# Optimization experiments

Measured on AMD Instinct MI355X. Metric: run time of the kernel, lower is better.

Reference implementation:

```python
import jax, jax.numpy as jnp
import numpy as np

H = 128            # hidden_size; also the chunk length from torch.split(x, hidden_size)
NUM_CHUNKS = 4096  # B
INPUT_SIZE = 1
NUM_CLASSES = 1


def setup_inputs() -> dict:
    key = jax.random.key(0)
    ks = jax.random.split(key, 7)
    N = NUM_CHUNKS * H
    s = 1.0 / np.sqrt(H).astype(np.float32)
    x = jax.random.normal(ks[0], (N,), dtype=jnp.float32)
    W_ih = jax.random.uniform(ks[1], (4 * H, INPUT_SIZE), minval=-s, maxval=s, dtype=jnp.float32)
    W_hh = jax.random.uniform(ks[2], (4 * H, H), minval=-s, maxval=s, dtype=jnp.float32)
    b_ih = jax.random.uniform(ks[3], (4 * H,), minval=-s, maxval=s, dtype=jnp.float32)
    b_hh = jax.random.uniform(ks[4], (4 * H,), minval=-s, maxval=s, dtype=jnp.float32)
    fc_W = jax.random.uniform(ks[5], (NUM_CLASSES, H), minval=-s, maxval=s, dtype=jnp.float32)
    fc_b = jax.random.uniform(ks[6], (NUM_CLASSES,), minval=-s, maxval=s, dtype=jnp.float32)
    return {"x": x, "W_ih": W_ih, "W_hh": W_hh, "b_ih": b_ih, "b_hh": b_hh,
            "fc_W": fc_W, "fc_b": fc_b}


def reference(x, W_ih, W_hh, b_ih, b_hh, fc_W, fc_b):
    # Original: split flat x into chunks of length H, run each chunk as a
    # batch-1 LSTM (input_size=1), take final hidden state, apply fc_out.
    # Here all chunks are batched into one fused recurrent pass.
    Hh = W_hh.shape[1]
    xb = x.reshape(-1, Hh, 1)                                  # [B, T=H, 1]
    # input projection is time-parallel: precompute gate pre-activations
    pre = jnp.einsum('bti,gi->btg', xb, W_ih) + b_ih + b_hh    # [B, T, 4H]

    def step(carry, p_t):
        h, c = carry                                           # [B, H] each
        gates = p_t + h @ W_hh.T                               # [B, 4H]
        i, f, g, o = jnp.split(gates, 4, axis=-1)              # PyTorch gate order i,f,g,o
        i = jax.nn.sigmoid(i)
        f = jax.nn.sigmoid(f)
        g = jnp.tanh(g)
        o = jax.nn.sigmoid(o)
        c = f * c + i * g
        h = o * jnp.tanh(c)
        return (h, c), None

    B = xb.shape[0]
    h0 = jnp.zeros((B, Hh), dtype=x.dtype)
    c0 = jnp.zeros((B, Hh), dtype=x.dtype)
    (hT, _), _ = jax.lax.scan(step, (h0, c0), jnp.swapaxes(pre, 0, 1))
    return hT @ fc_W.T + fc_b                                  # [B, num_classes]
```

## Files before the change

### kernel.cpp

```cpp
#include <hip/hip_runtime.h>


#define H   128
#define T   128
#define BLOCK 512
#define HSTRIDE 136
#define XSTRIDE 20
#define LOG2E    1.44269504088896340736f
#define TWOLOG2E 2.88539008177792681472f

typedef _Float16 f16x8 __attribute__((ext_vector_type(8)));
typedef float    f32x4 __attribute__((ext_vector_type(4)));

__global__ void prep_whh_kernel(const float* __restrict__ W_hh, _Float16* __restrict__ wfrag)
{
    int idx = blockIdx.x * blockDim.x + threadIdx.x;
    int l15 =  idx        & 15;
    int q   = (idx >> 4)  & 3;
    int kc  = (idx >> 6)  & 3;
    int g   = (idx >> 8)  & 3;
    int ct  = (idx >> 10) & 7;
    int n  = g * H + ct * 16 + l15;
    int k0 = kc * 32 + q * 8;
    float s = (g == 2) ? TWOLOG2E : LOG2E;
    const float* src = W_hh + (size_t)n * H + k0;
    f16x8 f;
    #pragma unroll
    for (int i = 0; i < 8; ++i) f[i] = (_Float16)(src[i] * s);
    *(f16x8*)(wfrag + (size_t)idx * 8) = f;
}

__device__ __forceinline__ float frcp(float v)  { return __builtin_amdgcn_rcpf(v); }
__device__ __forceinline__ float fexp2(float v) { return __builtin_amdgcn_exp2f(v); }

__device__ __forceinline__ void lstm_step(const _Float16* hr, _Float16* hw,
                                          const float* xp,
                                          const f16x8 wf[4][4],
                                          const float* wihs, const float* biass,
                                          float* c, int l15, int q, int jcol)
{
    const _Float16* ar = hr + l15 * HSTRIDE + q * 8;
    f16x8 af0 = *(const f16x8*)(ar);
    f16x8 af1 = *(const f16x8*)(ar + 32);
    f16x8 af2 = *(const f16x8*)(ar + 64);
    f16x8 af3 = *(const f16x8*)(ar + 96);

    float4 xl = *(const float4*)xp;
    f32x4 acc[4];
    #pragma unroll
    for (int g = 0; g < 4; ++g) {
        f32x4 iv;
        iv[0] = fmaf(xl.x, wihs[g], biass[g]);
        iv[1] = fmaf(xl.y, wihs[g], biass[g]);
        iv[2] = fmaf(xl.z, wihs[g], biass[g]);
        iv[3] = fmaf(xl.w, wihs[g], biass[g]);
        acc[g] = __builtin_amdgcn_mfma_f32_16x16x32_f16(af0, wf[g][0], iv, 0, 0, 0);
    }
    #pragma unroll
    for (int g = 0; g < 4; ++g)
        acc[g] = __builtin_amdgcn_mfma_f32_16x16x32_f16(af1, wf[g][1], acc[g], 0, 0, 0);
    #pragma unroll
    for (int g = 0; g < 4; ++g)
        acc[g] = __builtin_amdgcn_mfma_f32_16x16x32_f16(af2, wf[g][2], acc[g], 0, 0, 0);
    #pragma unroll
    for (int g = 0; g < 4; ++g)
        acc[g] = __builtin_amdgcn_mfma_f32_16x16x32_f16(af3, wf[g][3], acc[g], 0, 0, 0);

    float Ei[4], Ef[4], Eg[4], Eo[4];
    #pragma unroll
    for (int r = 0; r < 4; ++r) {
        Ei[r] = fexp2(-acc[0][r]);
        Ef[r] = fexp2(-acc[1][r]);
        Eg[r] = fexp2( acc[2][r]);
        Eo[r] = fexp2(-acc[3][r]);
    }
    _Float16* hwp = hw + (q * 4) * HSTRIDE + jcol;
    #pragma unroll
    for (int r = 0; r < 4; ++r) {
        float u  = 1.0f + Ei[r];
        float v  = 1.0f + Ef[r];
        float w  = 1.0f + Eg[r];
        float wm = Eg[r] - 1.0f;
        float uw = u * w;
        float cn = fmaf(c[r], uw, wm * v) * frcp(v * uw);
        c[r] = cn;
        float Ec = fexp2(cn * TWOLOG2E);
        float hv = (Ec - 1.0f) * frcp((Ec + 1.0f) * (1.0f + Eo[r]));
        hwp[r * HSTRIDE] = (_Float16)hv;
    }
}

__launch_bounds__(BLOCK, 2)
__global__ void lstm_fused_kernel(const float* __restrict__ x,
                                  const float* __restrict__ W_ih,
                                  const _Float16* __restrict__ wfrag,
                                  const float* __restrict__ b_ih,
                                  const float* __restrict__ b_hh,
                                  const float* __restrict__ fc_W,
                                  const float* __restrict__ fc_b,
                                  float* __restrict__ out)
{
    __shared__ __align__(16) float xs[T][XSTRIDE];
    __shared__ __align__(16) _Float16 hb0[16 * HSTRIDE];
    __shared__ __align__(16) _Float16 hb1[16 * HSTRIDE];

    const int tid  = threadIdx.x;
    const int wave = tid >> 6;
    const int lane = tid & 63;
    const int l15  = lane & 15;
    const int q    = lane >> 4;
    const int jcol = wave * 16 + l15;

    {
        const int t0 = tid & 127;
        const int bb = tid >> 7;
        const float* xb = x + (size_t)blockIdx.x * (16 * T);
        xs[t0][bb]      = xb[bb * T + t0];
        xs[t0][bb + 4]  = xb[(bb + 4) * T + t0];
        xs[t0][bb + 8]  = xb[(bb + 8) * T + t0];
        xs[t0][bb + 12] = xb[(bb + 12) * T + t0];
    }
    for (int i = tid; i < 16 * HSTRIDE; i += BLOCK)
        hb0[i] = (_Float16)0.0f;

    f16x8 wf[4][4];
    float wihs[4], biass[4];
    {
        const _Float16* wbase = wfrag + (size_t)wave * 8192;
        #pragma unroll
        for (int g = 0; g < 4; ++g) {
            const int n = g * H + jcol;
            const float s = (g == 2) ? TWOLOG2E : LOG2E;
            wihs[g]  = W_ih[n] * s;
            biass[g] = (b_ih[n] + b_hh[n]) * s;
            #pragma unroll
            for (int kc = 0; kc < 4; ++kc)
                wf[g][kc] = *(const f16x8*)(wbase + ((((g * 4 + kc) * 4 + q) * 16 + l15) * 8));
        }
    }

    float c[4] = {0.f, 0.f, 0.f, 0.f};
    const float* xp = &xs[0][q * 4];

    __syncthreads();

    #pragma unroll 1
    for (int t2 = 0; t2 < T / 2; ++t2) {
        lstm_step(hb0, hb1, xp, wf, wihs, biass, c, l15, q, jcol);
        xp += XSTRIDE;
        __syncthreads();
        lstm_step(hb1, hb0, xp, wf, wihs, biass, c, l15, q, jcol);
        xp += XSTRIDE;
        __syncthreads();
    }

    if (tid < 256) {
        const int b    = tid >> 4;
        const int part = tid & 15;
        const _Float16* hrow = &hb0[b * HSTRIDE];
        float s = 0.0f;
        #pragma unroll
        for (int i = 0; i < 8; ++i) {
            const int j = part * 8 + i;
            s += fc_W[j] * (float)hrow[j];
        }
        s += __shfl_xor(s, 8, 16);
        s += __shfl_xor(s, 4, 16);
        s += __shfl_xor(s, 2, 16);
        s += __shfl_xor(s, 1, 16);
        if (part == 0)
            out[blockIdx.x * 16 + b] = s + fc_b[0];
    }
}

extern "C" void kernel_launch(void* const* d_in, const int* in_sizes, int n_in,
                              void* d_out, int out_size, void* d_ws, size_t ws_size,
                              hipStream_t stream)
{
    const float* x    = (const float*)d_in[0];
    const float* W_ih = (const float*)d_in[1];
    const float* W_hh = (const float*)d_in[2];
    const float* b_ih = (const float*)d_in[3];
    const float* b_hh = (const float*)d_in[4];
    const float* fc_W = (const float*)d_in[5];
    const float* fc_b = (const float*)d_in[6];
    float* out = (float*)d_out;

    _Float16* wfrag = (_Float16*)d_ws;

    hipLaunchKernelGGL(prep_whh_kernel, dim3(32), dim3(256), 0, stream, W_hh, wfrag);

    const int B = in_sizes[0] / H;
    dim3 grid(B / 16);
    dim3 block(BLOCK);
    hipLaunchKernelGGL(lstm_fused_kernel, grid, block, 0, stream,
                       x, W_ih, wfrag, b_ih, b_hh, fc_W, fc_b, out);
}
```

Baseline: 168.9 us.

## Interleave two 16-sequence cohorts per block to overlap MFMA and gate math

Each block now processes 32 sequences split into two cohorts, A and B, with separate hidden-state buffers and cell states. The recurrence is software-pipelined so the MFMA gate matmul of one cohort is issued next to the elementwise sigmoid/tanh update of the other. The aim is to hide MFMA latency and the barrier behind independent VALU work. In exchange the grid is halved, so with 4096 sequences only 128 blocks launch. That may leave half of the GPU's compute units idle, and per-thread register and LDS use grows.

```diff
diff --git a/kernel.cpp b/kernel.cpp
--- a/kernel.cpp
+++ b/kernel.cpp
@@ -3,9 +3,10 @@
 
 #define H   128
 #define T   128
+#define MB  32
 #define BLOCK 512
 #define HSTRIDE 136
-#define XSTRIDE 20
+#define XSTRIDE 36
 #define LOG2E    1.44269504088896340736f
 #define TWOLOG2E 2.88539008177792681472f
 
@@ -33,11 +34,11 @@
 __device__ __forceinline__ float frcp(float v)  { return __builtin_amdgcn_rcpf(v); }
 __device__ __forceinline__ float fexp2(float v) { return __builtin_amdgcn_exp2f(v); }
 
-__device__ __forceinline__ void lstm_step(const _Float16* hr, _Float16* hw,
-                                          const float* xp,
-                                          const f16x8 wf[4][4],
-                                          const float* wihs, const float* biass,
-                                          float* c, int l15, int q, int jcol)
+__device__ __forceinline__ void mfma_coh(f32x4 acc[4], const _Float16* hr,
+                                         const float* xp,
+                                         const f16x8 wf[4][4],
+                                         const float* wihs, const float* biass,
+                                         int l15, int q)
 {
     const _Float16* ar = hr + l15 * HSTRIDE + q * 8;
     f16x8 af0 = *(const f16x8*)(ar);
@@ -46,7 +47,6 @@
     f16x8 af3 = *(const f16x8*)(ar + 96);
 
     float4 xl = *(const float4*)xp;
-    f32x4 acc[4];
     #pragma unroll
     for (int g = 0; g < 4; ++g) {
         f32x4 iv;
@@ -65,7 +65,11 @@
     #pragma unroll
     for (int g = 0; g < 4; ++g)
         acc[g] = __builtin_amdgcn_mfma_f32_16x16x32_f16(af3, wf[g][3], acc[g], 0, 0, 0);
-
+}
+
+__device__ __forceinline__ void ew_coh(const f32x4 acc[4], float* c, _Float16* hw,
+                                       int q, int jcol)
+{
     float Ei[4], Ef[4], Eg[4], Eo[4];
     #pragma unroll
     for (int r = 0; r < 4; ++r) {
@@ -101,8 +105,8 @@
                                   float* __restrict__ out)
 {
     __shared__ __align__(16) float xs[T][XSTRIDE];
-    __shared__ __align__(16) _Float16 hb0[16 * HSTRIDE];
-    __shared__ __align__(16) _Float16 hb1[16 * HSTRIDE];
+    __shared__ __align__(16) _Float16 hA[16 * HSTRIDE];
+    __shared__ __align__(16) _Float16 hB[16 * HSTRIDE];
 
     const int tid  = threadIdx.x;
     const int wave = tid >> 6;
@@ -113,15 +117,18 @@
 
     {
         const int t0 = tid & 127;
-        const int bb = tid >> 7;
-        const float* xb = x + (size_t)blockIdx.x * (16 * T);
-        xs[t0][bb]      = xb[bb * T + t0];
-        xs[t0][bb + 4]  = xb[(bb + 4) * T + t0];
-        xs[t0][bb + 8]  = xb[(bb + 8) * T + t0];
-        xs[t0][bb + 12] = xb[(bb + 12) * T + t0];
-    }
-    for (int i = tid; i < 16 * HSTRIDE; i += BLOCK)
-        hb0[i] = (_Float16)0.0f;
+        const int b0 = tid >> 7;
+        const float* xb = x + (size_t)blockIdx.x * (MB * T);
+        #pragma unroll
+        for (int i = 0; i < 8; ++i) {
+            const int b = b0 + 4 * i;
+            xs[t0][b] = xb[b * T + t0];
+        }
+    }
+    for (int i = tid; i < 16 * HSTRIDE; i += BLOCK) {
+        hA[i] = (_Float16)0.0f;
+        hB[i] = (_Float16)0.0f;
+    }
 
     f16x8 wf[4][4];
     float wihs[4], biass[4];
@@ -139,25 +146,35 @@
         }
     }
 
-    float c[4] = {0.f, 0.f, 0.f, 0.f};
-    const float* xp = &xs[0][q * 4];
-
+    float cA[4] = {0.f, 0.f, 0.f, 0.f};
+    float cB[4] = {0.f, 0.f, 0.f, 0.f};
+    f32x4 accA[4], accB[4];
+    const int xq = q * 4;
+
+    __syncthreads();
+
+    mfma_coh(accA, hA, &xs[0][xq], wf, wihs, biass, l15, q);
+    __syncthreads();
+    mfma_coh(accB, hB, &xs[0][16 + xq], wf, wihs, biass, l15, q);
+    ew_coh(accA, cA, hA, q, jcol);
     __syncthreads();
 
     #pragma unroll 1
-    for (int t2 = 0; t2 < T / 2; ++t2) {
-        lstm_step(hb0, hb1, xp, wf, wihs, biass, c, l15, q, jcol);
-        xp += XSTRIDE;
+    for (int t = 1; t < T; ++t) {
+        mfma_coh(accA, hA, &xs[t][xq], wf, wihs, biass, l15, q);
+        ew_coh(accB, cB, hB, q, jcol);
         __syncthreads();
-        lstm_step(hb1, hb0, xp, wf, wihs, biass, c, l15, q, jcol);
-        xp += XSTRIDE;
+        mfma_coh(accB, hB, &xs[t][16 + xq], wf, wihs, biass, l15, q);
+        ew_coh(accA, cA, hA, q, jcol);
         __syncthreads();
     }
-
-    if (tid < 256) {
+    ew_coh(accB, cB, hB, q, jcol);
+    __syncthreads();
+
+    {
         const int b    = tid >> 4;
         const int part = tid & 15;
-        const _Float16* hrow = &hb0[b * HSTRIDE];
+        const _Float16* hrow = (b < 16) ? &hA[b * HSTRIDE] : &hB[(b - 16) * HSTRIDE];
         float s = 0.0f;
         #pragma unroll
         for (int i = 0; i < 8; ++i) {
@@ -169,7 +186,7 @@
         s += __shfl_xor(s, 2, 16);
         s += __shfl_xor(s, 1, 16);
         if (part == 0)
-            out[blockIdx.x * 16 + b] = s + fc_b[0];
+            out[blockIdx.x * MB + b] = s + fc_b[0];
     }
 }
 
@@ -191,7 +208,7 @@
     hipLaunchKernelGGL(prep_whh_kernel, dim3(32), dim3(256), 0, stream, W_hh, wfrag);
 
     const int B = in_sizes[0] / H;
-    dim3 grid(B / 16);
+    dim3 grid(B / MB);
     dim3 block(BLOCK);
     hipLaunchKernelGGL(lstm_fused_kernel, grid, block, 0, stream,
                        x, W_ih, wfrag, b_ih, b_hh, fc_W, fc_b, out);
```

After: 262.6 us. 1.55x slower.

## Halve block size and assign two hidden-column tiles per wave

Applied to the files above, without the earlier changes.

The LSTM block shrinks from 8 to 4 waves. Each wave now keeps W_hh fragments for two 16-column tiles in registers and issues 8 independent MFMA chains per K-slice instead of 4. The aim is cheaper per-step barriers and more instruction-level parallelism within a wave. The cost is about twice the weight registers per lane, and the SIMDs lose the second wave that could overlap one wave's MFMA work with another's gate math.

```diff
diff --git a/kernel.cpp b/kernel.cpp
--- a/kernel.cpp
+++ b/kernel.cpp
@@ -3,7 +3,7 @@
 
 #define H   128
 #define T   128
-#define BLOCK 512
+#define BLOCK 256
 #define HSTRIDE 136
 #define XSTRIDE 20
 #define LOG2E    1.44269504088896340736f
@@ -35,9 +35,9 @@
 
 __device__ __forceinline__ void lstm_step(const _Float16* hr, _Float16* hw,
                                           const float* xp,
-                                          const f16x8 wf[4][4],
-                                          const float* wihs, const float* biass,
-                                          float* c, int l15, int q, int jcol)
+                                          const f16x8 wf[2][4][4],
+                                          const float wihs[2][4], const float biass[2][4],
+                                          float c[2][4], int l15, int q, int jc0)
 {
     const _Float16* ar = hr + l15 * HSTRIDE + q * 8;
     f16x8 af0 = *(const f16x8*)(ar);
@@ -46,47 +46,58 @@
     f16x8 af3 = *(const f16x8*)(ar + 96);
 
     float4 xl = *(const float4*)xp;
-    f32x4 acc[4];
-    #pragma unroll
-    for (int g = 0; g < 4; ++g) {
-        f32x4 iv;
-        iv[0] = fmaf(xl.x, wihs[g], biass[g]);
-        iv[1] = fmaf(xl.y, wihs[g], biass[g]);
-        iv[2] = fmaf(xl.z, wihs[g], biass[g]);
-        iv[3] = fmaf(xl.w, wihs[g], biass[g]);
-        acc[g] = __builtin_amdgcn_mfma_f32_16x16x32_f16(af0, wf[g][0], iv, 0, 0, 0);
-    }
-    #pragma unroll
-    for (int g = 0; g < 4; ++g)
-        acc[g] = __builtin_amdgcn_mfma_f32_16x16x32_f16(af1, wf[g][1], acc[g], 0, 0, 0);
-    #pragma unroll
-    for (int g = 0; g < 4; ++g)
-        acc[g] = __builtin_amdgcn_mfma_f32_16x16x32_f16(af2, wf[g][2], acc[g], 0, 0, 0);
-    #pragma unroll
-    for (int g = 0; g < 4; ++g)
-        acc[g] = __builtin_amdgcn_mfma_f32_16x16x32_f16(af3, wf[g][3], acc[g], 0, 0, 0);
-
-    float Ei[4], Ef[4], Eg[4], Eo[4];
-    #pragma unroll
-    for (int r = 0; r < 4; ++r) {
-        Ei[r] = fexp2(-acc[0][r]);
-        Ef[r] = fexp2(-acc[1][r]);
-        Eg[r] = fexp2( acc[2][r]);
-        Eo[r] = fexp2(-acc[3][r]);
-    }
-    _Float16* hwp = hw + (q * 4) * HSTRIDE + jcol;
-    #pragma unroll
-    for (int r = 0; r < 4; ++r) {
-        float u  = 1.0f + Ei[r];
-        float v  = 1.0f + Ef[r];
-        float w  = 1.0f + Eg[r];
-        float wm = Eg[r] - 1.0f;
-        float uw = u * w;
-        float cn = fmaf(c[r], uw, wm * v) * frcp(v * uw);
-        c[r] = cn;
-        float Ec = fexp2(cn * TWOLOG2E);
-        float hv = (Ec - 1.0f) * frcp((Ec + 1.0f) * (1.0f + Eo[r]));
-        hwp[r * HSTRIDE] = (_Float16)hv;
+    f32x4 acc[2][4];
+    #pragma unroll
+    for (int ct = 0; ct < 2; ++ct)
+        #pragma unroll
+        for (int g = 0; g < 4; ++g) {
+            f32x4 iv;
+            iv[0] = fmaf(xl.x, wihs[ct][g], biass[ct][g]);
+            iv[1] = fmaf(xl.y, wihs[ct][g], biass[ct][g]);
+            iv[2] = fmaf(xl.z, wihs[ct][g], biass[ct][g]);
+            iv[3] = fmaf(xl.w, wihs[ct][g], biass[ct][g]);
+            acc[ct][g] = __builtin_amdgcn_mfma_f32_16x16x32_f16(af0, wf[ct][g][0], iv, 0, 0, 0);
+        }
+    #pragma unroll
+    for (int ct = 0; ct < 2; ++ct)
+        #pragma unroll
+        for (int g = 0; g < 4; ++g)
+            acc[ct][g] = __builtin_amdgcn_mfma_f32_16x16x32_f16(af1, wf[ct][g][1], acc[ct][g], 0, 0, 0);
+    #pragma unroll
+    for (int ct = 0; ct < 2; ++ct)
+        #pragma unroll
+        for (int g = 0; g < 4; ++g)
+            acc[ct][g] = __builtin_amdgcn_mfma_f32_16x16x32_f16(af2, wf[ct][g][2], acc[ct][g], 0, 0, 0);
+    #pragma unroll
+    for (int ct = 0; ct < 2; ++ct)
+        #pragma unroll
+        for (int g = 0; g < 4; ++g)
+            acc[ct][g] = __builtin_amdgcn_mfma_f32_16x16x32_f16(af3, wf[ct][g][3], acc[ct][g], 0, 0, 0);
+
+    #pragma unroll
+    for (int ct = 0; ct < 2; ++ct) {
+        float Ei[4], Ef[4], Eg[4], Eo[4];
+        #pragma unroll
+        for (int r = 0; r < 4; ++r) {
+            Ei[r] = fexp2(-acc[ct][0][r]);
+            Ef[r] = fexp2(-acc[ct][1][r]);
+            Eg[r] = fexp2( acc[ct][2][r]);
+            Eo[r] = fexp2(-acc[ct][3][r]);
+        }
+        _Float16* hwp = hw + (q * 4) * HSTRIDE + jc0 + ct * 16;
+        #pragma unroll
+        for (int r = 0; r < 4; ++r) {
+            float u  = 1.0f + Ei[r];
+            float v  = 1.0f + Ef[r];
+            float w  = 1.0f + Eg[r];
+            float wm = Eg[r] - 1.0f;
+            float uw = u * w;
+            float cn = fmaf(c[ct][r], uw, wm * v) * frcp(v * uw);
+            c[ct][r] = cn;
+            float Ec = fexp2(cn * TWOLOG2E);
+            float hv = (Ec - 1.0f) * frcp((Ec + 1.0f) * (1.0f + Eo[r]));
+            hwp[r * HSTRIDE] = (_Float16)hv;
+        }
     }
 }
 
@@ -109,52 +120,53 @@
     const int lane = tid & 63;
     const int l15  = lane & 15;
     const int q    = lane >> 4;
-    const int jcol = wave * 16 + l15;
+    const int jc0  = wave * 32 + l15;
 
     {
         const int t0 = tid & 127;
-        const int bb = tid >> 7;
+        const int bb = (tid >> 7) * 8;
         const float* xb = x + (size_t)blockIdx.x * (16 * T);
-        xs[t0][bb]      = xb[bb * T + t0];
-        xs[t0][bb + 4]  = xb[(bb + 4) * T + t0];
-        xs[t0][bb + 8]  = xb[(bb + 8) * T + t0];
-        xs[t0][bb + 12] = xb[(bb + 12) * T + t0];
+        #pragma unroll
+        for (int i = 0; i < 8; ++i)
+            xs[t0][bb + i] = xb[(bb + i) * T + t0];
     }
     for (int i = tid; i < 16 * HSTRIDE; i += BLOCK)
         hb0[i] = (_Float16)0.0f;
 
-    f16x8 wf[4][4];
-    float wihs[4], biass[4];
-    {
-        const _Float16* wbase = wfrag + (size_t)wave * 8192;
+    f16x8 wf[2][4][4];
+    float wihs[2][4], biass[2][4];
+    #pragma unroll
+    for (int ct = 0; ct < 2; ++ct) {
+        const _Float16* wbase = wfrag + (size_t)(wave * 2 + ct) * 8192;
         #pragma unroll
         for (int g = 0; g < 4; ++g) {
-            const int n = g * H + jcol;
+            const int n = g * H + wave * 32 + ct * 16 + l15;
             const float s = (g == 2) ? TWOLOG2E : LOG2E;
-            wihs[g]  = W_ih[n] * s;
-            biass[g] = (b_ih[n] + b_hh[n]) * s;
+            wihs[ct][g]  = W_ih[n] * s;
+            biass[ct][g] = (b_ih[n] + b_hh[n]) * s;
             #pragma unroll
             for (int kc = 0; kc < 4; ++kc)
-                wf[g][kc] = *(const f16x8*)(wbase + ((((g * 4 + kc) * 4 + q) * 16 + l15) * 8));
-        }
-    }
-
-    float c[4] = {0.f, 0.f, 0.f, 0.f};
+                wf[ct][g][kc] = *(const f16x8*)(wbase + ((((g * 4 + kc) * 4 + q) * 16 + l15) * 8));
+        }
+    }
+
+    float c[2][4] = {{0.f, 0.f, 0.f, 0.f}, {0.f, 0.f, 0.f, 0.f}};
+
+    __syncthreads();
+
     const float* xp = &xs[0][q * 4];
-
-    __syncthreads();
 
     #pragma unroll 1
     for (int t2 = 0; t2 < T / 2; ++t2) {
-        lstm_step(hb0, hb1, xp, wf, wihs, biass, c, l15, q, jcol);
+        lstm_step(hb0, hb1, xp, wf, wihs, biass, c, l15, q, jc0);
         xp += XSTRIDE;
         __syncthreads();
-        lstm_step(hb1, hb0, xp, wf, wihs, biass, c, l15, q, jcol);
+        lstm_step(hb1, hb0, xp, wf, wihs, biass, c, l15, q, jc0);
         xp += XSTRIDE;
         __syncthreads();
     }
 
-    if (tid < 256) {
+    {
         const int b    = tid >> 4;
         const int part = tid & 15;
         const _Float16* hrow = &hb0[b * HSTRIDE];
```

Result: slower. 173.2 us (+2.5%).
